# Kernel optimization log

Hardware: AMD Instinct MI355X
Metric: run time of the kernel (lower is better)

Reference implementation:

```python
import jax, jax.numpy as jnp
import numpy as np

TW = 25          # time_window
H = 128          # hidden_features
NL = 6           # hidden_layer
N = 8192         # batch*n_nodes
E = 131072       # edges (avg degree 16)
EDGE_DIM = 51    # 50 (u diff) + 1 (pos_x diff)
LEM_IN = 4       # pos_x, u_ch0, u_ch1, ts
PDE_L = 16.0
PDE_TMAX = 4.0
PDE_DT = 0.04
NEG_SLOPE = 0.2  # PyG GATConv leaky_relu slope


def swish(x):
    return x * jax.nn.sigmoid(x)


def setup_inputs() -> dict:
    key = jax.random.key(0)
    ks = jax.random.split(key, 32)
    def p(k, shape, s=0.05):
        return jax.random.normal(k, shape, jnp.float32) * s
    inp = {}
    inp['u'] = jax.random.normal(ks[0], (N, 2 * TW), jnp.float32)
    inp['pos'] = jax.random.uniform(ks[1], (N, 2), jnp.float32)
    inp['edge_index'] = jax.random.randint(ks[2], (2, E), 0, N)
    # LEM cell params (inp2hid: 4H, hid2hid: 3H, transform_z: H)
    inp['lem_inp_w'] = p(ks[3], (4 * H, LEM_IN)); inp['lem_inp_b'] = jnp.zeros(4 * H, jnp.float32)
    inp['lem_hid_w'] = p(ks[4], (3 * H, H));      inp['lem_hid_b'] = jnp.zeros(3 * H, jnp.float32)
    inp['lem_z_w'] = p(ks[5], (H, H));            inp['lem_z_b'] = jnp.zeros(H, jnp.float32)
    # lemoutput_mlp
    inp['mlp1_w'] = p(ks[6], (H, H)); inp['mlp1_b'] = jnp.zeros(H, jnp.float32)
    inp['mlp2_w'] = p(ks[7], (H, H)); inp['mlp2_b'] = jnp.zeros(H, jnp.float32)
    # main GAT layers (stacked over NL)
    inp['gnn_lin_w'] = p(ks[8], (NL, H, H)); inp['gnn_edge_w'] = p(ks[9], (NL, H, EDGE_DIM))
    inp['gnn_att_src'] = p(ks[10], (NL, H)); inp['gnn_att_dst'] = p(ks[11], (NL, H))
    inp['gnn_att_edge'] = p(ks[12], (NL, H)); inp['gnn_bias'] = jnp.zeros((NL, H), jnp.float32)
    # gate GAT layers
    inp['gate_lin_w'] = p(ks[13], (NL, H, H)); inp['gate_edge_w'] = p(ks[14], (NL, H, EDGE_DIM))
    inp['gate_att_src'] = p(ks[15], (NL, H)); inp['gate_att_dst'] = p(ks[16], (NL, H))
    inp['gate_att_edge'] = p(ks[17], (NL, H)); inp['gate_bias'] = jnp.zeros((NL, H), jnp.float32)
    # double_mlp + conv1d decoder (time_window==25 branch)
    inp['dbl_w'] = p(ks[18], (2 * H, H)); inp['dbl_b'] = jnp.zeros(2 * H, jnp.float32)
    inp['conv1_w'] = p(ks[19], (8, 2, 16)); inp['conv1_b'] = jnp.zeros(8, jnp.float32)
    inp['conv2_w'] = p(ks[20], (2, 8, 14)); inp['conv2_b'] = jnp.zeros(2, jnp.float32)
    return inp


def _gat(x, src, dst, edge_attr, lin_w, edge_w, a_src, a_dst, a_edge, bias):
    """Single-head GATConv with edge features (PyG semantics, aggregate at dst)."""
    xt = x @ lin_w.T                      # [N,H]
    et = edge_attr @ edge_w.T             # [E,H]
    logits = jax.nn.leaky_relu((xt @ a_src)[src] + (xt @ a_dst)[dst] + et @ a_edge, NEG_SLOPE)
    amax = jax.ops.segment_max(logits, dst, num_segments=N)
    amax = jnp.where(jnp.isfinite(amax), amax, 0.0)
    ex = jnp.exp(logits - amax[dst])
    denom = jax.ops.segment_sum(ex, dst, num_segments=N)
    w = ex / (denom[dst] + 1e-16)         # edge softmax over incoming edges
    out = jax.ops.segment_sum(w[:, None] * xt[src], dst, num_segments=N)
    return out + bias


def _forward(u, pos, lem_inp_w, lem_inp_b, lem_hid_w, lem_hid_b, lem_z_w, lem_z_b,
             mlp1_w, mlp1_b, mlp2_w, mlp2_b,
             gnn_lin_w, gnn_edge_w, gnn_att_src, gnn_att_dst, gnn_att_edge, gnn_bias,
             gate_lin_w, gate_edge_w, gate_att_src, gate_att_dst, gate_att_edge, gate_bias,
             dbl_w, dbl_b, conv1_w, conv1_b, conv2_w, conv2_b, edge_index):
    pos_x = pos[:, 1:2] / PDE_L    # [N,1]
    pos_t = pos[:, 0:1] / PDE_TMAX # [N,1]
    dt = jnp.cumsum(jnp.full((TW,), PDE_DT, jnp.float32))  # [TW]
    ts = pos_t + dt[None, :]       # [N,TW]
    # LEM input: [TW, N, 4] = (pos_x, u channel 0, u channel 1, ts)
    lem_x = jnp.concatenate([
        jnp.broadcast_to(pos_x[None, :, :], (TW, N, 1)),
        u[:, :TW].T[:, :, None],
        u[:, TW:].T[:, :, None],
        ts.T[:, :, None],
    ], axis=-1)

    def cell(carry, xt):
        y, z = carry
        ii = xt @ lem_inp_w.T + lem_inp_b   # [N,4H]
        hh = y @ lem_hid_w.T + lem_hid_b    # [N,3H]
        i1, i2, i3, i4 = jnp.split(ii, 4, axis=-1)
        h1, h2, h3 = jnp.split(hh, 3, axis=-1)
        ms_dt_bar = jax.nn.sigmoid(i1 + h1)
        ms_dt = jax.nn.sigmoid(i2 + h2)
        z = (1.0 - ms_dt) * z + ms_dt * jnp.tanh(i3 + h3)
        y = (1.0 - ms_dt_bar) * y + ms_dt_bar * jnp.tanh(z @ lem_z_w.T + lem_z_b + i4)
        return (y, z), None

    y0 = jnp.zeros((N, H), u.dtype)
    (y, _), _ = jax.lax.scan(cell, (y0, y0), lem_x)
    h = swish(y @ mlp1_w.T + mlp1_b)
    h = swish(h @ mlp2_w.T + mlp2_b)

    src, dst = edge_index[0], edge_index[1]
    edge_attr = jnp.concatenate([u[src] - u[dst], pos_x[src] - pos_x[dst]], axis=-1)  # [E,51]

    for i in range(NL):
        tau = jax.nn.sigmoid(_gat(h, src, dst, edge_attr, gate_lin_w[i], gate_edge_w[i],
                                  gate_att_src[i], gate_att_dst[i], gate_att_edge[i], gate_bias[i]))
        msg = swish(_gat(h, src, dst, edge_attr, gnn_lin_w[i], gnn_edge_w[i],
                         gnn_att_src[i], gnn_att_dst[i], gnn_att_edge[i], gnn_bias[i]))
        h = (1.0 - tau) * h + tau * msg

    h2 = swish(h @ dbl_w.T + dbl_b).reshape(N, 2, H)  # [N,2,128]
    dn = ('NCH', 'OIH', 'NCH')
    d = jax.lax.conv_general_dilated(h2, conv1_w, (3,), 'VALID', dimension_numbers=dn)
    d = swish(d + conv1_b[None, :, None])              # [N,8,38]
    d = jax.lax.conv_general_dilated(d, conv2_w, (1,), 'VALID', dimension_numbers=dn)
    d = d + conv2_b[None, :, None]                     # [N,2,25]
    out = u.reshape(N, 2, TW) + dt[None, None, :] * d
    return out.reshape(N, 2 * TW)


def reference(u, pos, edge_index, lem_inp_w, lem_inp_b, lem_hid_w, lem_hid_b, lem_z_w, lem_z_b,
              mlp1_w, mlp1_b, mlp2_w, mlp2_b,
              gnn_lin_w, gnn_edge_w, gnn_att_src, gnn_att_dst, gnn_att_edge, gnn_bias,
              gate_lin_w, gate_edge_w, gate_att_src, gate_att_dst, gate_att_edge, gate_bias,
              dbl_w, dbl_b, conv1_w, conv1_b, conv2_w, conv2_b):
    return _forward(u, pos, lem_inp_w, lem_inp_b, lem_hid_w, lem_hid_b, lem_z_w, lem_z_b,
                    mlp1_w, mlp1_b, mlp2_w, mlp2_b,
                    gnn_lin_w, gnn_edge_w, gnn_att_src, gnn_att_dst, gnn_att_edge, gnn_bias,
                    gate_lin_w, gate_edge_w, gate_att_src, gate_att_dst, gate_att_edge, gate_bias,
                    dbl_w, dbl_b, conv1_w, conv1_b, conv2_w, conv2_b, edge_index)
```

## Files before the change

### kernel.cpp

```cpp
#include <hip/hip_runtime.h>
#include <hip/hip_cooperative_groups.h>

#define N_NODES 8192
#define N_EDGES 131072

namespace cg = cooperative_groups;

using short8 = __attribute__((ext_vector_type(8))) short;
using f32x4  = __attribute__((ext_vector_type(4))) float;

__device__ __forceinline__ float rcpf(float x){ return __builtin_amdgcn_rcpf(x); }
__device__ __forceinline__ float sigm(float x){ return rcpf(1.0f+__expf(-x)); }
__device__ __forceinline__ float ftanh(float x){ float e=__expf(2.0f*x); return (e-1.0f)*rcpf(e+1.0f); }
__device__ __forceinline__ float swishf(float x){ return x*sigm(x); }
__device__ __forceinline__ float leaky(float x){ return x>=0.0f? x : 0.2f*x; }
__device__ __forceinline__ float dot4(float4 a, float4 b){ return a.x*b.x+a.y*b.y+a.z*b.z+a.w*b.w; }
__device__ __forceinline__ short f2bf(float x){
  unsigned u=__float_as_uint(x);
  unsigned r=(u + 0x7fffu + ((u>>16)&1u))>>16;
  return (short)r;
}
__device__ __forceinline__ int cvtpk(float a, float b){
  int r; asm("v_cvt_pk_bf16_f32 %0, %1, %2" : "=v"(r) : "v"(a), "v"(b)); return r;
}

__device__ __forceinline__ float wave_rsum(float v){
  #pragma unroll
  for(int m=32;m;m>>=1) v+=__shfl_xor(v,m);
  return v;
}

__global__ __launch_bounds__(256) void hist_kernel(const int* __restrict__ dst, int* __restrict__ cnt){
  int e=blockIdx.x*256+threadIdx.x;
  if(e<N_EDGES) atomicAdd(&cnt[dst[e]],1);
}

__global__ __launch_bounds__(1024) void scan_kernel(const int* __restrict__ cnt, int* __restrict__ rowptr, int* __restrict__ cursor){
  __shared__ int sums[1024];
  int t=threadIdx.x; int base=t*8;
  int local[8]; int s=0;
  #pragma unroll
  for(int i=0;i<8;++i){ local[i]=s; s+=cnt[base+i]; }
  sums[t]=s; __syncthreads();
  for(int off=1;off<1024;off<<=1){
    int v=(t>=off)?sums[t-off]:0;
    __syncthreads();
    sums[t]+=v;
    __syncthreads();
  }
  int offset=(t>0)?sums[t-1]:0;
  #pragma unroll
  for(int i=0;i<8;++i){ int v=offset+local[i]; rowptr[base+i]=v; cursor[base+i]=v; }
  if(t==1023) rowptr[N_NODES]=sums[1023];
}

__global__ __launch_bounds__(256) void scatter_kernel(const int* __restrict__ src, const int* __restrict__ dst,
                                                      int* __restrict__ cursor, int* __restrict__ csr_src){
  int e=blockIdx.x*256+threadIdx.x;
  if(e<N_EDGES){
    int slot=atomicAdd(&cursor[dst[e]],1);
    csr_src[slot]=src[e];
  }
}

__global__ __launch_bounds__(256) void prep_bf16_kernel(
    const float* __restrict__ lem_hid_w, const float* __restrict__ lem_z_w,
    const float* __restrict__ mlp1_w, const float* __restrict__ mlp2_w,
    const float* __restrict__ gate_lin_w, const float* __restrict__ gnn_lin_w,
    const float* __restrict__ gate_ew, const float* __restrict__ gnn_ew,
    const float* __restrict__ gate_ae, const float* __restrict__ gnn_ae,
    short* __restrict__ whb, short* __restrict__ wzb, short* __restrict__ w1b,
    short* __restrict__ w2b, short* __restrict__ wlin16, float* __restrict__ we)
{
  int i=blockIdx.x*256+threadIdx.x;
  if(i<49152){ whb[i]=f2bf(lem_hid_w[i]); return; }
  if(i<65536){ int k=i-49152; wzb[k]=f2bf(lem_z_w[k]); return; }
  if(i<81920){ int k=i-65536; w1b[k]=f2bf(mlp1_w[k]); return; }
  if(i<98304){ int k=i-81920; w2b[k]=f2bf(mlp2_w[k]); return; }
  if(i<294912){
    int k=i-98304;
    int l=k>>15, which=(k>>14)&1, r=k&16383;
    const float* s = which? gnn_lin_w + l*16384 + r : gate_lin_w + l*16384 + r;
    wlin16[k]=f2bf(*s);
    return;
  }
  int idx=i-294912;
  if(idx>=12*51) return;
  int g=idx/51, k=idx%51, l=g>>1;
  const float* ew = (g&1)? gnn_ew + l*128*51 : gate_ew + l*128*51;
  const float* ae = (g&1)? gnn_ae + l*128    : gate_ae + l*128;
  float s=0.f;
  for(int f=0;f<128;++f) s+=ew[f*51+k]*ae[f];
  we[idx]=s;
}

__global__ __launch_bounds__(128) void gsc_kernel(const float* __restrict__ u, const float* __restrict__ pos,
                                                  const float* __restrict__ we, float* __restrict__ gsc){
  int n=blockIdx.x*128+threadIdx.x;
  float uv[50];
  #pragma unroll
  for(int k=0;k<50;++k) uv[k]=u[n*50+k];
  float px=pos[n*2+1]*(1.0f/16.0f);
  for(int g=0;g<12;++g){
    const float* w=we+g*51;
    float s=w[50]*px;
    #pragma unroll
    for(int k=0;k<50;++k) s+=w[k]*uv[k];
    gsc[g*N_NODES+n]=s;
  }
}

__device__ __forceinline__ void transform_phase(
    int tid, int n0,
    const short* __restrict__ h16, short* __restrict__ xts,
    float* __restrict__ ssred, float* __restrict__ sdred,
    const short* __restrict__ wl,
    const float* __restrict__ a_sg, const float* __restrict__ a_dg,
    const float* __restrict__ a_sm, const float* __restrict__ a_dm,
    const float* __restrict__ gsc_g, const float* __restrict__ gsc_m,
    short* __restrict__ xt_out, float* __restrict__ ss_out, float* __restrict__ sd_out)
{
  const int lane=tid&63, w=tid>>6;
  const int cg_=w&1, ch=w>>1;
  const int r16=lane&15, kq=lane>>4;
  __syncthreads();
  short8 afr[4];
  #pragma unroll
  for(int kk=0;kk<4;++kk)
    afr[kk]=*(const short8*)&h16[r16*128 + ((kk*32+kq*8) ^ ((r16&7)<<3))];
  const short* wb = wl + cg_*16384;
  const float* as_ = cg_? a_sm : a_sg;
  const float* ad_ = cg_? a_dm : a_dg;
  float ssp[4]={0,0,0,0}, sdp[4]={0,0,0,0};
  #pragma unroll
  for(int ci=0;ci<2;++ci){
    int c0=(ch*2+ci)*16;
    f32x4 acc={0.f,0.f,0.f,0.f};
    #pragma unroll
    for(int kk=0;kk<4;++kk){
      short8 b=*(const short8*)(wb + (c0+r16)*128 + kk*32 + kq*8);
      acc=__builtin_amdgcn_mfma_f32_16x16x32_bf16(afr[kk],b,acc,0,0,0);
    }
    float av=as_[c0+r16], dv=ad_[c0+r16];
    #pragma unroll
    for(int r=0;r<4;++r){
      ssp[r]+=acc[r]*av; sdp[r]+=acc[r]*dv;
      xts[(kq*4+r)*256 + cg_*128 + c0 + r16]=f2bf(acc[r]);
    }
  }
  #pragma unroll
  for(int m=1;m<16;m<<=1){
    #pragma unroll
    for(int r=0;r<4;++r){ ssp[r]+=__shfl_xor(ssp[r],m); sdp[r]+=__shfl_xor(sdp[r],m); }
  }
  if(r16==0){
    #pragma unroll
    for(int r=0;r<4;++r){ ssred[w*16+kq*4+r]=ssp[r]; sdred[w*16+kq*4+r]=sdp[r]; }
  }
  __syncthreads();
  if(tid<32){
    int node=tid&15, cg2=tid>>4;
    float sv=0.f, dv=0.f;
    #pragma unroll
    for(int c2=0;c2<4;++c2){ sv+=ssred[(c2*2+cg2)*16+node]; dv+=sdred[(c2*2+cg2)*16+node]; }
    float gv=(cg2? gsc_m:gsc_g)[n0+node];
    ss_out[2*(n0+node)+cg2]=sv+gv;
    sd_out[2*(n0+node)+cg2]=dv-gv;
  }
  {
    const short8* sp=(const short8*)xts;
    short8* dp=(short8*)(xt_out + (size_t)n0*256);
    dp[tid]=sp[tid];
  }
}

__device__ __forceinline__ float4 aggregate_node(
    int n, int lane, float4* __restrict__ stgw,
    const int* __restrict__ rowptr, const int* __restrict__ csr_src,
    const short* __restrict__ xt_in, const float* __restrict__ ss_in, const float* __restrict__ sd_in,
    const float* __restrict__ bias_g, const float* __restrict__ bias_m,
    const float* __restrict__ hrow)
{
  const int s0=rowptr[n], deg=rowptr[n+1]-s0;
  const float2 sdv=*(const float2*)(sd_in+2*n);
  const float bg=sdv.x, bm=sdv.y;
  float dg=0.f,dm=0.f, acc0=0.f,acc1=0.f,acc2=0.f,acc3=0.f;
  for(int c=0;c<deg;c+=64){
    int i=c+lane, s=0; float eg=0.f, em=0.f;
    if(i<deg){
      s=csr_src[s0+i];
      float2 ssv=*(const float2*)(ss_in+2*s);
      eg=__expf(fminf(leaky(ssv.x+bg),60.f));
      em=__expf(fminf(leaky(ssv.y+bm),60.f));
      dg+=eg; dm+=em;
    }
    float4 st; st.x=__int_as_float(s); st.y=eg; st.z=em; st.w=0.f;
    stgw[lane]=st;
    __threadfence_block();
    int cnt=min(64,deg-c);
    for(int cb=0;cb<cnt;cb+=8){
      int sj[8]; float wj[8];
      #pragma unroll
      for(int j=0;j<8;++j){
        int idx=cb+j;
        float4 ev=stgw[idx<cnt? idx : cb];
        sj[j]=__float_as_int(ev.x);
        wj[j]=(idx<cnt)? (lane<32? ev.y : ev.z) : 0.f;
      }
      uint2 rows[8];
      #pragma unroll
      for(int j=0;j<8;++j)
        rows[j]=*(const uint2*)(xt_in + (size_t)sj[j]*256 + 4*lane);
      #pragma unroll
      for(int j=0;j<8;++j){
        float wv=wj[j];
        unsigned p0=rows[j].x, p1=rows[j].y;
        acc0+=wv*__uint_as_float(p0<<16);
        acc1+=wv*__uint_as_float(p0&0xffff0000u);
        acc2+=wv*__uint_as_float(p1<<16);
        acc3+=wv*__uint_as_float(p1&0xffff0000u);
      }
    }
  }
  dg=wave_rsum(dg); dm=wave_rsum(dm);
  float rr = lane<32? rcpf(dg+1e-16f) : rcpf(dm+1e-16f);
  const float* bp = lane<32? bias_g+4*lane : bias_m+4*(lane-32);
  float4 bv=*(const float4*)bp;
  float o0=acc0*rr+bv.x, o1=acc1*rr+bv.y, o2=acc2*rr+bv.z, o3=acc3*rr+bv.w;
  float s0_=sigm(o0), s1_=sigm(o1), s2_=sigm(o2), s3_=sigm(o3);
  float v0=lane<32? s0_:o0*s0_;
  float v1=lane<32? s1_:o1*s1_;
  float v2=lane<32? s2_:o2*s2_;
  float v3=lane<32? s3_:o3*s3_;
  float m0=__shfl_xor(v0,32), m1=__shfl_xor(v1,32), m2=__shfl_xor(v2,32), m3=__shfl_xor(v3,32);
  float4 r;
  if(lane<32){
    float4 hv=*(const float4*)(hrow + 4*lane);
    r.x=(1.0f-v0)*hv.x+v0*m0;
    r.y=(1.0f-v1)*hv.y+v1*m1;
    r.z=(1.0f-v2)*hv.z+v2*m2;
    r.w=(1.0f-v3)*hv.w+v3*m3;
  } else { r.x=r.y=r.z=r.w=0.f; }
  return r;
}

__global__ __launch_bounds__(512,2) void lem_t0_kernel(
    const float* __restrict__ u, const float* __restrict__ pos,
    const float* __restrict__ Wi, const float* __restrict__ bi,
    const short* __restrict__ whb, const float* __restrict__ bh,
    const short* __restrict__ wzb, const float* __restrict__ bz,
    const short* __restrict__ w1b, const float* __restrict__ b1,
    const short* __restrict__ w2b, const float* __restrict__ b2,
    float* __restrict__ hout,
    const short* __restrict__ wl,
    const float* __restrict__ a_sg, const float* __restrict__ a_dg,
    const float* __restrict__ a_sm, const float* __restrict__ a_dm,
    const float* __restrict__ gsc_g, const float* __restrict__ gsc_m,
    short* __restrict__ xt_out, float* __restrict__ ss_out, float* __restrict__ sd_out)
{
  __shared__ short y16[2][16*128];
  __shared__ short z16[2][16*128];
  __shared__ float u_s[32*50];
  __shared__ short h16[16*128];
  __shared__ short xts[16*256];
  __shared__ float ssred[128], sdred[128];

  const int tid=threadIdx.x, lane=tid&63, w=tid>>6;
  const int node=lane&15, q=lane>>4;
  const int n7=node&7;
  const int n0=blockIdx.x*32;

  for(int i=tid;i<32*50;i+=512) u_s[i]=u[n0*50+i];
  for(int i=tid;i<2*16*64;i+=512) ((int*)y16)[i]=0;

  const float px0=pos[(n0+node)*2+1]*(1.0f/16.0f),    pt0=pos[(n0+node)*2+0]*0.25f;
  const float px1=pos[(n0+16+node)*2+1]*(1.0f/16.0f), pt1=pos[(n0+16+node)*2+0]*0.25f;

  float bb[4][4], wix[4][4], wiw[4][4], wiy[4][4], wiz[4][4];
  #pragma unroll
  for(int gg=0; gg<4; ++gg){
    #pragma unroll
    for(int r=0;r<4;++r){
      int fr = w*16+q*4+r;
      int row = gg*128+fr;
      float4 wi = *(const float4*)(Wi+4*row);
      bb[gg][r] = bi[row] + ((gg<3)? bh[row] : bz[fr]);
      wix[gg][r]=wi.x; wiw[gg][r]=wi.w; wiy[gg][r]=wi.y; wiz[gg][r]=wi.z;
    }
  }

  short8 whf[3][4];
  #pragma unroll
  for(int gg=0;gg<3;++gg)
    #pragma unroll
    for(int kk=0;kk<4;++kk)
      whf[gg][kk]=*(const short8*)(whb + (gg*128 + w*16 + node)*128 + kk*32 + q*8);
  short8 wzf[4];
  #pragma unroll
  for(int kk=0;kk<4;++kk)
    wzf[kk]=*(const short8*)(wzb + (w*16 + node)*128 + kk*32 + q*8);

  float yr0[4]={0.f,0.f,0.f,0.f}, zr0[4]={0.f,0.f,0.f,0.f};
  float yr1[4]={0.f,0.f,0.f,0.f}, zr1[4]={0.f,0.f,0.f,0.f};
  float msb0[4], i4s0[4], msb1[4], i4s1[4];
  const int wrslot = (w*16+q*4) ^ (n7<<3);
  const int rdbase = n7<<3;
  __syncthreads();

  for(int t=0;t<25;++t){
    const float tf=(float)(t+1);
    {
      f32x4 h1a={0.f,0.f,0.f,0.f}, h2a=h1a, h3a=h1a;
      #pragma unroll
      for(int kk=0;kk<4;++kk){
        short8 yb=*(const short8*)&y16[0][node*128 + ((kk*32 + q*8) ^ rdbase)];
        h1a=__builtin_amdgcn_mfma_f32_16x16x32_bf16(whf[0][kk],yb,h1a,0,0,0);
        h2a=__builtin_amdgcn_mfma_f32_16x16x32_bf16(whf[1][kk],yb,h2a,0,0,0);
        h3a=__builtin_amdgcn_mfma_f32_16x16x32_bf16(whf[2][kk],yb,h3a,0,0,0);
      }
      const float u0=u_s[node*50+t], u1=u_s[node*50+25+t];
      const float ts=pt0+0.04f*tf;
      #pragma unroll
      for(int r=0;r<4;++r){
        float i1=bb[0][r]+wix[0][r]*px0+wiw[0][r]*ts+wiy[0][r]*u0+wiz[0][r]*u1;
        float i2=bb[1][r]+wix[1][r]*px0+wiw[1][r]*ts+wiy[1][r]*u0+wiz[1][r]*u1;
        float i3=bb[2][r]+wix[2][r]*px0+wiw[2][r]*ts+wiy[2][r]*u0+wiz[2][r]*u1;
        i4s0[r] =bb[3][r]+wix[3][r]*px0+wiw[3][r]*ts+wiy[3][r]*u0+wiz[3][r]*u1;
        msb0[r]=sigm(i1+h1a[r]);
        float ms=sigm(i2+h2a[r]);
        zr0[r]=(1.0f-ms)*zr0[r]+ms*ftanh(i3+h3a[r]);
      }
      int2 zz; zz.x=cvtpk(zr0[0],zr0[1]); zz.y=cvtpk(zr0[2],zr0[3]);
      *(int2*)&z16[0][node*128 + wrslot]=zz;
    }
    {
      f32x4 h1a={0.f,0.f,0.f,0.f}, h2a=h1a, h3a=h1a;
      #pragma unroll
      for(int kk=0;kk<4;++kk){
        short8 yb=*(const short8*)&y16[1][node*128 + ((kk*32 + q*8) ^ rdbase)];
        h1a=__builtin_amdgcn_mfma_f32_16x16x32_bf16(whf[0][kk],yb,h1a,0,0,0);
        h2a=__builtin_amdgcn_mfma_f32_16x16x32_bf16(whf[1][kk],yb,h2a,0,0,0);
        h3a=__builtin_amdgcn_mfma_f32_16x16x32_bf16(whf[2][kk],yb,h3a,0,0,0);
      }
      const float u0=u_s[(16+node)*50+t], u1=u_s[(16+node)*50+25+t];
      const float ts=pt1+0.04f*tf;
      #pragma unroll
      for(int r=0;r<4;++r){
        float i1=bb[0][r]+wix[0][r]*px1+wiw[0][r]*ts+wiy[0][r]*u0+wiz[0][r]*u1;
        float i2=bb[1][r]+wix[1][r]*px1+wiw[1][r]*ts+wiy[1][r]*u0+wiz[1][r]*u1;
        float i3=bb[2][r]+wix[2][r]*px1+wiw[2][r]*ts+wiy[2][r]*u0+wiz[2][r]*u1;
        i4s1[r] =bb[3][r]+wix[3][r]*px1+wiw[3][r]*ts+wiy[3][r]*u0+wiz[3][r]*u1;
        msb1[r]=sigm(i1+h1a[r]);
        float ms=sigm(i2+h2a[r]);
        zr1[r]=(1.0f-ms)*zr1[r]+ms*ftanh(i3+h3a[r]);
      }
      int2 zz; zz.x=cvtpk(zr1[0],zr1[1]); zz.y=cvtpk(zr1[2],zr1[3]);
      *(int2*)&z16[1][node*128 + wrslot]=zz;
    }
    __syncthreads();
    {
      f32x4 zw={0.f,0.f,0.f,0.f};
      #pragma unroll
      for(int kk=0;kk<4;++kk){
        short8 zb=*(const short8*)&z16[0][node*128 + ((kk*32 + q*8) ^ rdbase)];
        zw=__builtin_amdgcn_mfma_f32_16x16x32_bf16(wzf[kk],zb,zw,0,0,0);
      }
      #pragma unroll
      for(int r=0;r<4;++r)
        yr0[r]=(1.0f-msb0[r])*yr0[r]+msb0[r]*ftanh(zw[r]+i4s0[r]);
      int2 yy; yy.x=cvtpk(yr0[0],yr0[1]); yy.y=cvtpk(yr0[2],yr0[3]);
      *(int2*)&y16[0][node*128 + wrslot]=yy;
    }
    {
      f32x4 zw={0.f,0.f,0.f,0.f};
      #pragma unroll
      for(int kk=0;kk<4;++kk){
        short8 zb=*(const short8*)&z16[1][node*128 + ((kk*32 + q*8) ^ rdbase)];
        zw=__builtin_amdgcn_mfma_f32_16x16x32_bf16(wzf[kk],zb,zw,0,0,0);
      }
      #pragma unroll
      for(int r=0;r<4;++r)
        yr1[r]=(1.0f-msb1[r])*yr1[r]+msb1[r]*ftanh(zw[r]+i4s1[r]);
      int2 yy; yy.x=cvtpk(yr1[0],yr1[1]); yy.y=cvtpk(yr1[2],yr1[3]);
      *(int2*)&y16[1][node*128 + wrslot]=yy;
    }
    __syncthreads();
  }

  #pragma unroll
  for(int nt=0;nt<2;++nt){
    {
      short8 w1f[4];
      #pragma unroll
      for(int kk=0;kk<4;++kk)
        w1f[kk]=*(const short8*)(w1b + (w*16 + node)*128 + kk*32 + q*8);
      float4 b1v=*(const float4*)(b1 + w*16 + q*4);
      f32x4 a={0.f,0.f,0.f,0.f};
      #pragma unroll
      for(int kk=0;kk<4;++kk){
        short8 yb=*(const short8*)&y16[nt][node*128 + ((kk*32 + q*8) ^ rdbase)];
        a=__builtin_amdgcn_mfma_f32_16x16x32_bf16(w1f[kk],yb,a,0,0,0);
      }
      float t0=swishf(a[0]+b1v.x), t1=swishf(a[1]+b1v.y);
      float t2=swishf(a[2]+b1v.z), t3=swishf(a[3]+b1v.w);
      int2 zz; zz.x=cvtpk(t0,t1); zz.y=cvtpk(t2,t3);
      *(int2*)&z16[nt][node*128 + wrslot]=zz;
    }
    __syncthreads();
    {
      short8 w2f[4];
      #pragma unroll
      for(int kk=0;kk<4;++kk)
        w2f[kk]=*(const short8*)(w2b + (w*16 + node)*128 + kk*32 + q*8);
      float4 b2v=*(const float4*)(b2 + w*16 + q*4);
      f32x4 a={0.f,0.f,0.f,0.f};
      #pragma unroll
      for(int kk=0;kk<4;++kk){
        short8 zb=*(const short8*)&z16[nt][node*128 + ((kk*32 + q*8) ^ rdbase)];
        a=__builtin_amdgcn_mfma_f32_16x16x32_bf16(w2f[kk],zb,a,0,0,0);
      }
      float h0=swishf(a[0]+b2v.x), h1=swishf(a[1]+b2v.y);
      float h2=swishf(a[2]+b2v.z), h3=swishf(a[3]+b2v.w);
      float4 hv; hv.x=h0; hv.y=h1; hv.z=h2; hv.w=h3;
      *(float4*)(hout + (size_t)(n0+nt*16+node)*128 + w*16+q*4)=hv;
      int2 hb; hb.x=cvtpk(h0,h1); hb.y=cvtpk(h2,h3);
      *(int2*)&h16[node*128 + wrslot]=hb;
    }
    transform_phase(tid,n0+nt*16,h16,xts,ssred,sdred,wl,a_sg,a_dg,a_sm,a_dm,gsc_g,gsc_m,xt_out,ss_out,sd_out);
  }
}

__global__ __launch_bounds__(512,2) void gnn_persist_kernel(
    const int* __restrict__ rowptr, const int* __restrict__ csr_src,
    const float* __restrict__ hin,
    short* __restrict__ xtA, float* __restrict__ ssA, float* __restrict__ sdA,
    short* __restrict__ xtB, float* __restrict__ ssB, float* __restrict__ sdB,
    const short* __restrict__ wlin16,
    const float* __restrict__ gate_att_src, const float* __restrict__ gate_att_dst,
    const float* __restrict__ gnn_att_src, const float* __restrict__ gnn_att_dst,
    const float* __restrict__ gsc,
    const float* __restrict__ gate_bias, const float* __restrict__ gnn_bias,
    const float* __restrict__ u,
    const float* __restrict__ Wd, const float* __restrict__ bd,
    const float* __restrict__ w1, const float* __restrict__ b1,
    const float* __restrict__ w2, const float* __restrict__ b2,
    float* __restrict__ out)
{
  __shared__ float hfp[32*128];
  __shared__ union SM {
    struct {
      short h16[16*128];
      short xts[16*256];
      float ssred[128], sdred[128];
      float4 stg[8][64];
    } g;
    struct {
      float h2[16][2][128];
      float c1[16][8][38];
      float w1s[256], w2s[224], b1s[8], b2s[2];
    } d;
  } sm;

  cg::grid_group grid = cg::this_grid();
  const int tid=threadIdx.x, lane=tid&63, w=tid>>6;
  const int n0=blockIdx.x*32;

  for(int i=tid;i<32*128;i+=512) hfp[i]=hin[(size_t)n0*128+i];
  __syncthreads();

  for(int l=0;l<6;++l){
    const short* xt_in = (l&1)? xtB : xtA;
    const float* ss_in = (l&1)? ssB : ssA;
    const float* sd_in = (l&1)? sdB : sdA;
    const float* bias_g = gate_bias + l*128;
    const float* bias_m = gnn_bias + l*128;
    #pragma unroll
    for(int nt=0;nt<2;++nt){
      #pragma unroll
      for(int which=0;which<2;++which){
        int rl=w*2+which;
        int row=nt*16+rl;
        int n=n0+row;
        float4 hv=aggregate_node(n,lane,sm.g.stg[w],rowptr,csr_src,xt_in,ss_in,sd_in,bias_g,bias_m,&hfp[row*128]);
        if(lane<32){
          *(float4*)&hfp[row*128+4*lane]=hv;
          int2 hb; hb.x=cvtpk(hv.x,hv.y); hb.y=cvtpk(hv.z,hv.w);
          *(int2*)&sm.g.h16[rl*128 + ((4*lane) ^ ((rl&7)<<3))]=hb;
        }
      }
      if(l<5){
        int lp=l+1;
        transform_phase(tid,n0+nt*16,sm.g.h16,sm.g.xts,sm.g.ssred,sm.g.sdred,
          wlin16+(size_t)lp*32768,
          gate_att_src+lp*128, gate_att_dst+lp*128,
          gnn_att_src+lp*128, gnn_att_dst+lp*128,
          gsc+(size_t)(2*lp)*N_NODES, gsc+(size_t)(2*lp+1)*N_NODES,
          (l&1)? xtA:xtB, (l&1)? ssA:ssB, (l&1)? sdA:sdB);
      }
    }
    if(l<5){
      __threadfence();
      grid.sync();
      __threadfence();
    }
  }

  __syncthreads();
  if(tid<256) sm.d.w1s[tid]=w1[tid];
  else if(tid<480) sm.d.w2s[tid-256]=w2[tid-256];
  else if(tid<488) sm.d.b1s[tid-480]=b1[tid-480];
  else if(tid<490) sm.d.b2s[tid-488]=b2[tid-488];
  __syncthreads();
  for(int nt=0;nt<2;++nt){
    const float* hbase=&hfp[nt*16*128];
    {
      int o=tid&255, grp=tid>>8;
      const float4* wp=(const float4*)(Wd + o*128);
      float acc[8];
      #pragma unroll
      for(int n=0;n<8;++n) acc[n]=0.f;
      for(int k=0;k<32;++k){
        float4 wv=wp[k];
        #pragma unroll
        for(int n=0;n<8;++n){ float4 hval=*(const float4*)&hbase[(grp*8+n)*128+k*4]; acc[n]+=dot4(wv,hval); }
      }
      float bdv=bd[o];
      int chn=o>>7, p=o&127;
      #pragma unroll
      for(int n=0;n<8;++n) sm.d.h2[grp*8+n][chn][p]=swishf(acc[n]+bdv);
    }
    __syncthreads();
    for(int idx=tid; idx<16*8*38; idx+=512){
      int n=idx/(8*38); int r=idx%(8*38); int oc=r/38, p=r%38;
      float acc=sm.d.b1s[oc];
      const float* ww=&sm.d.w1s[oc*32];
      #pragma unroll
      for(int ic=0;ic<2;++ic)
        #pragma unroll
        for(int k=0;k<16;++k) acc+=ww[ic*16+k]*sm.d.h2[n][ic][3*p+k];
      sm.d.c1[n][oc][p]=swishf(acc);
    }
    __syncthreads();
    for(int idx=tid; idx<16*2*25; idx+=512){
      int n=idx/50; int r=idx%50; int oc=r/25, p=r%25;
      float acc=sm.d.b2s[oc];
      const float* ww=&sm.d.w2s[oc*112];
      #pragma unroll
      for(int ic=0;ic<8;++ic)
        #pragma unroll
        for(int k=0;k<14;++k) acc+=ww[ic*14+k]*sm.d.c1[n][ic][p+k];
      int col=oc*25+p;
      int gn=n0+nt*16+n;
      out[gn*50+col]=u[gn*50+col]+0.04f*(float)(p+1)*acc;
    }
    __syncthreads();
  }
}

__global__ __launch_bounds__(512,2) void gat_fused_kernel(
    const int* __restrict__ rowptr, const int* __restrict__ csr_src,
    const short* __restrict__ xt_in, const float* __restrict__ ss_in, const float* __restrict__ sd_in,
    const float* __restrict__ bias_g, const float* __restrict__ bias_m,
    float* __restrict__ h,
    const short* __restrict__ wl,
    const float* __restrict__ a_sg, const float* __restrict__ a_dg,
    const float* __restrict__ a_sm, const float* __restrict__ a_dm,
    const float* __restrict__ gsc_g, const float* __restrict__ gsc_m,
    short* __restrict__ xt_out, float* __restrict__ ss_out, float* __restrict__ sd_out)
{
  __shared__ short h16[16*128];
  __shared__ short xts[16*256];
  __shared__ float ssred[128], sdred[128];
  __shared__ float4 stg[8][64];
  const int tid=threadIdx.x, lane=tid&63, w=tid>>6;
  const int n0=blockIdx.x*16;
  #pragma unroll
  for(int which=0;which<2;++which){
    int row=w*2+which, n=n0+row;
    float4 hv=aggregate_node(n,lane,stg[w],rowptr,csr_src,xt_in,ss_in,sd_in,bias_g,bias_m,h+(size_t)n*128);
    if(lane<32){
      *(float4*)(h+(size_t)n*128+4*lane)=hv;
      int2 hb; hb.x=cvtpk(hv.x,hv.y); hb.y=cvtpk(hv.z,hv.w);
      *(int2*)&h16[row*128 + ((4*lane) ^ ((row&7)<<3))]=hb;
    }
  }
  transform_phase(tid,n0,h16,xts,ssred,sdred,wl,a_sg,a_dg,a_sm,a_dm,gsc_g,gsc_m,xt_out,ss_out,sd_out);
}

__global__ __launch_bounds__(512,2) void gat_last_decoder_kernel(
    const int* __restrict__ rowptr, const int* __restrict__ csr_src,
    const short* __restrict__ xt_in, const float* __restrict__ ss_in, const float* __restrict__ sd_in,
    const float* __restrict__ bias_g, const float* __restrict__ bias_m,
    const float* __restrict__ h, const float* __restrict__ u,
    const float* __restrict__ Wd, const float* __restrict__ bd,
    const float* __restrict__ w1, const float* __restrict__ b1,
    const float* __restrict__ w2, const float* __restrict__ b2,
    float* __restrict__ out)
{
  __shared__ float hdec[16*128];
  __shared__ float h2[16][2][128];
  __shared__ float c1[16][8][38];
  __shared__ float w1s[256], w2s[224], b1s[8], b2s[2];
  __shared__ float4 stg[8][64];
  const int tid=threadIdx.x, lane=tid&63, w=tid>>6;
  const int n0=blockIdx.x*16;
  if(tid<256) w1s[tid]=w1[tid];
  else if(tid<480) w2s[tid-256]=w2[tid-256];
  else if(tid<488) b1s[tid-480]=b1[tid-480];
  else if(tid<490) b2s[tid-488]=b2[tid-488];
  #pragma unroll
  for(int which=0;which<2;++which){
    int row=w*2+which, n=n0+row;
    float4 hv=aggregate_node(n,lane,stg[w],rowptr,csr_src,xt_in,ss_in,sd_in,bias_g,bias_m,h+(size_t)n*128);
    if(lane<32) *(float4*)&hdec[row*128+4*lane]=hv;
  }
  __syncthreads();
  {
    int o=tid&255, grp=tid>>8;
    const float4* wp=(const float4*)(Wd + o*128);
    float acc[8];
    #pragma unroll
    for(int n=0;n<8;++n) acc[n]=0.f;
    for(int k=0;k<32;++k){
      float4 wv=wp[k];
      #pragma unroll
      for(int n=0;n<8;++n){ float4 hval=*(const float4*)&hdec[(grp*8+n)*128+k*4]; acc[n]+=dot4(wv,hval); }
    }
    float bdv=bd[o];
    int chn=o>>7, p=o&127;
    #pragma unroll
    for(int n=0;n<8;++n) h2[grp*8+n][chn][p]=swishf(acc[n]+bdv);
  }
  __syncthreads();
  for(int idx=tid; idx<16*8*38; idx+=512){
    int n=idx/(8*38); int r=idx%(8*38); int oc=r/38, p=r%38;
    float acc=b1s[oc];
    const float* ww=&w1s[oc*32];
    #pragma unroll
    for(int ic=0;ic<2;++ic)
      #pragma unroll
      for(int k=0;k<16;++k) acc+=ww[ic*16+k]*h2[n][ic][3*p+k];
    c1[n][oc][p]=swishf(acc);
  }
  __syncthreads();
  for(int idx=tid; idx<16*2*25; idx+=512){
    int n=idx/50; int r=idx%50; int oc=r/25, p=r%25;
    float acc=b2s[oc];
    const float* ww=&w2s[oc*112];
    #pragma unroll
    for(int ic=0;ic<8;++ic)
      #pragma unroll
      for(int k=0;k<14;++k) acc+=ww[ic*14+k]*c1[n][ic][p+k];
    int col=oc*25+p;
    out[(n0+n)*50+col]=u[(n0+n)*50+col]+0.04f*(float)(p+1)*acc;
  }
}

extern "C" void kernel_launch(void* const* d_in, const int* in_sizes, int n_in,
                              void* d_out, int out_size, void* d_ws, size_t ws_size,
                              hipStream_t stream)
{
  const float* u          =(const float*)d_in[0];
  const float* pos        =(const float*)d_in[1];
  const int*   ei         =(const int*)d_in[2];
  const float* lem_inp_w  =(const float*)d_in[3];
  const float* lem_inp_b  =(const float*)d_in[4];
  const float* lem_hid_w  =(const float*)d_in[5];
  const float* lem_hid_b  =(const float*)d_in[6];
  const float* lem_z_w    =(const float*)d_in[7];
  const float* lem_z_b    =(const float*)d_in[8];
  const float* mlp1_w     =(const float*)d_in[9];
  const float* mlp1_b     =(const float*)d_in[10];
  const float* mlp2_w     =(const float*)d_in[11];
  const float* mlp2_b     =(const float*)d_in[12];
  const float* gnn_lin_w  =(const float*)d_in[13];
  const float* gnn_edge_w =(const float*)d_in[14];
  const float* gnn_att_src=(const float*)d_in[15];
  const float* gnn_att_dst=(const float*)d_in[16];
  const float* gnn_att_edge=(const float*)d_in[17];
  const float* gnn_bias   =(const float*)d_in[18];
  const float* gate_lin_w =(const float*)d_in[19];
  const float* gate_edge_w=(const float*)d_in[20];
  const float* gate_att_src=(const float*)d_in[21];
  const float* gate_att_dst=(const float*)d_in[22];
  const float* gate_att_edge=(const float*)d_in[23];
  const float* gate_bias  =(const float*)d_in[24];
  const float* dbl_w      =(const float*)d_in[25];
  const float* dbl_b      =(const float*)d_in[26];
  const float* conv1_w    =(const float*)d_in[27];
  const float* conv1_b    =(const float*)d_in[28];
  const float* conv2_w    =(const float*)d_in[29];
  const float* conv2_b    =(const float*)d_in[30];
  float* out=(float*)d_out;

  char* ws=(char*)d_ws;
  size_t off=0;
  auto alloc=[&](size_t bytes)->char*{ char* p=ws+off; off+=(bytes+255)&~(size_t)255; return p; };
  float* h    =(float*)alloc((size_t)N_NODES*128*4);
  short* xtA  =(short*)alloc((size_t)N_NODES*256*2);
  short* xtB  =(short*)alloc((size_t)N_NODES*256*2);
  float* ssA  =(float*)alloc((size_t)N_NODES*2*4);
  float* ssB  =(float*)alloc((size_t)N_NODES*2*4);
  float* sdA  =(float*)alloc((size_t)N_NODES*2*4);
  float* sdB  =(float*)alloc((size_t)N_NODES*2*4);
  float* gsc  =(float*)alloc((size_t)12*N_NODES*4);
  float* wearr=(float*)alloc(12*51*4);
  int* cnt    =(int*)alloc(N_NODES*4);
  int* rowptr =(int*)alloc((N_NODES+8)*4);
  int* cursor =(int*)alloc(N_NODES*4);
  int* csrsrc =(int*)alloc((size_t)N_EDGES*4);
  short* whb  =(short*)alloc(384*128*2);
  short* wzb  =(short*)alloc(128*128*2);
  short* w1b  =(short*)alloc(128*128*2);
  short* w2b  =(short*)alloc(128*128*2);
  short* wlin16=(short*)alloc((size_t)6*2*128*128*2);

  const int* src=ei;
  const int* dst=ei+N_EDGES;

  hipMemsetAsync(cnt,0,N_NODES*4,stream);
  hist_kernel<<<N_EDGES/256,256,0,stream>>>(dst,cnt);
  scan_kernel<<<1,1024,0,stream>>>(cnt,rowptr,cursor);
  scatter_kernel<<<N_EDGES/256,256,0,stream>>>(src,dst,cursor,csrsrc);
  prep_bf16_kernel<<<(294912+612+255)/256,256,0,stream>>>(lem_hid_w,lem_z_w,mlp1_w,mlp2_w,
                                                      gate_lin_w,gnn_lin_w,
                                                      gate_edge_w,gnn_edge_w,gate_att_edge,gnn_att_edge,
                                                      whb,wzb,w1b,w2b,wlin16,wearr);
  gsc_kernel<<<N_NODES/128,128,0,stream>>>(u,pos,wearr,gsc);

  lem_t0_kernel<<<N_NODES/32,512,0,stream>>>(u,pos,lem_inp_w,lem_inp_b,whb,lem_hid_b,
      wzb,lem_z_b,w1b,mlp1_b,w2b,mlp2_b,h,
      wlin16,
      gate_att_src, gate_att_dst, gnn_att_src, gnn_att_dst,
      gsc, gsc+(size_t)N_NODES,
      xtA, ssA, sdA);

  int occ=0;
  hipError_t qerr=hipOccupancyMaxActiveBlocksPerMultiprocessor(&occ,
      reinterpret_cast<const void*>(gnn_persist_kernel), 512, 0);
  bool coop = (qerr==hipSuccess) && (occ>=1);

  if(coop){
    void* kargs[]={
      (void*)&rowptr,(void*)&csrsrc,(void*)&h,
      (void*)&xtA,(void*)&ssA,(void*)&sdA,
      (void*)&xtB,(void*)&ssB,(void*)&sdB,
      (void*)&wlin16,
      (void*)&gate_att_src,(void*)&gate_att_dst,(void*)&gnn_att_src,(void*)&gnn_att_dst,
      (void*)&gsc,
      (void*)&gate_bias,(void*)&gnn_bias,
      (void*)&u,(void*)&dbl_w,(void*)&dbl_b,
      (void*)&conv1_w,(void*)&conv1_b,(void*)&conv2_w,(void*)&conv2_b,
      (void*)&out
    };
    hipError_t lerr=hipLaunchCooperativeKernel((void*)gnn_persist_kernel,
        dim3(N_NODES/32), dim3(512), kargs, 0, stream);
    if(lerr==hipSuccess) return;
  }

  for(int l=0;l<5;++l){
    short* xin = (l&1)? xtB:xtA;  float* sin_=(l&1)? ssA:ssA;
    (void)xin; (void)sin_;
  }
  {
    short* xtbuf[2]={xtA,xtB};
    float* ssbuf[2]={ssA,ssB};
    float* sdbuf[2]={sdA,sdB};
    for(int l=0;l<5;++l){
      int in=l&1, o2=(l+1)&1;
      gat_fused_kernel<<<N_NODES/16,512,0,stream>>>(rowptr,csrsrc,
        xtbuf[in],ssbuf[in],sdbuf[in],
        gate_bias+l*128, gnn_bias+l*128, h,
        wlin16+(size_t)(l+1)*2*16384,
        gate_att_src+(l+1)*128, gate_att_dst+(l+1)*128,
        gnn_att_src+(l+1)*128, gnn_att_dst+(l+1)*128,
        gsc+(size_t)(2*(l+1))*N_NODES, gsc+(size_t)(2*(l+1)+1)*N_NODES,
        xtbuf[o2], ssbuf[o2], sdbuf[o2]);
    }
    gat_last_decoder_kernel<<<N_NODES/16,512,0,stream>>>(rowptr,csrsrc,
        xtbuf[1],ssbuf[1],sdbuf[1],
        gate_bias+5*128, gnn_bias+5*128, h, u,
        dbl_w, dbl_b, conv1_w, conv1_b, conv2_w, conv2_b, out);
  }
}
```

Measured before the change: 356.8 us.

## Halve nodes per persistent block, raise occupancy, and reorder gather before weight computation

The cooperative persistent GNN kernel now gives each block 16 nodes instead of 32, doubles the grid to 512 blocks, and sets launch bounds to 4 blocks per SM, which requires occupancy of at least 2 for the cooperative path. The aggregation loop stages source indices first and issues 16 row gathers per batch before computing the attention exponentials. This lets the exp/score latency overlap the outstanding gathers. It also splits the LDS staging into separate index and weight arrays. The tighter launch bounds may cause register spills, and if occupancy drops below 2 the code falls back to the multi-kernel path.

```diff
diff --git a/kernel.cpp b/kernel.cpp
--- a/kernel.cpp
+++ b/kernel.cpp
@@ -175,7 +175,7 @@
 }
 
 __device__ __forceinline__ float4 aggregate_node(
-    int n, int lane, float4* __restrict__ stgw,
+    int n, int lane, int* __restrict__ sidx, float2* __restrict__ wstg,
     const int* __restrict__ rowptr, const int* __restrict__ csr_src,
     const short* __restrict__ xt_in, const float* __restrict__ ss_in, const float* __restrict__ sd_in,
     const float* __restrict__ bias_g, const float* __restrict__ bias_m,
@@ -186,34 +186,36 @@
   const float bg=sdv.x, bm=sdv.y;
   float dg=0.f,dm=0.f, acc0=0.f,acc1=0.f,acc2=0.f,acc3=0.f;
   for(int c=0;c<deg;c+=64){
-    int i=c+lane, s=0; float eg=0.f, em=0.f;
-    if(i<deg){
-      s=csr_src[s0+i];
-      float2 ssv=*(const float2*)(ss_in+2*s);
-      eg=__expf(fminf(leaky(ssv.x+bg),60.f));
-      em=__expf(fminf(leaky(ssv.y+bm),60.f));
-      dg+=eg; dm+=em;
-    }
-    float4 st; st.x=__int_as_float(s); st.y=eg; st.z=em; st.w=0.f;
-    stgw[lane]=st;
+    int i=c+lane, s=0;
+    bool act=(i<deg);
+    if(act) s=csr_src[s0+i];
+    sidx[lane]= act? s : 0;
     __threadfence_block();
     int cnt=min(64,deg-c);
-    for(int cb=0;cb<cnt;cb+=8){
-      int sj[8]; float wj[8];
-      #pragma unroll
-      for(int j=0;j<8;++j){
+    for(int cb=0;cb<cnt;cb+=16){
+      uint2 rows[16];
+      #pragma unroll
+      for(int j=0;j<16;++j){
         int idx=cb+j;
-        float4 ev=stgw[idx<cnt? idx : cb];
-        sj[j]=__float_as_int(ev.x);
-        wj[j]=(idx<cnt)? (lane<32? ev.y : ev.z) : 0.f;
-      }
-      uint2 rows[8];
-      #pragma unroll
-      for(int j=0;j<8;++j)
-        rows[j]=*(const uint2*)(xt_in + (size_t)sj[j]*256 + 4*lane);
-      #pragma unroll
-      for(int j=0;j<8;++j){
-        float wv=wj[j];
+        int sj=sidx[idx<cnt? idx : cb];
+        rows[j]=*(const uint2*)(xt_in + (size_t)sj*256 + 4*lane);
+      }
+      if(cb==0){
+        float eg=0.f, em=0.f;
+        if(act){
+          float2 ssv=*(const float2*)(ss_in+2*s);
+          eg=__expf(fminf(leaky(ssv.x+bg),60.f));
+          em=__expf(fminf(leaky(ssv.y+bm),60.f));
+          dg+=eg; dm+=em;
+        }
+        wstg[lane]=make_float2(eg,em);
+        __threadfence_block();
+      }
+      #pragma unroll
+      for(int j=0;j<16;++j){
+        int idx=cb+j;
+        float2 wv2=wstg[idx<cnt? idx : cb];
+        float wv=(idx<cnt)? (lane<32? wv2.x : wv2.y) : 0.f;
         unsigned p0=rows[j].x, p1=rows[j].y;
         acc0+=wv*__uint_as_float(p0<<16);
         acc1+=wv*__uint_as_float(p0&0xffff0000u);
@@ -430,7 +432,7 @@
   }
 }
 
-__global__ __launch_bounds__(512,2) void gnn_persist_kernel(
+__global__ __launch_bounds__(512,4) void gnn_persist_kernel(
     const int* __restrict__ rowptr, const int* __restrict__ csr_src,
     const float* __restrict__ hin,
     short* __restrict__ xtA, float* __restrict__ ssA, float* __restrict__ sdA,
@@ -446,13 +448,14 @@
     const float* __restrict__ w2, const float* __restrict__ b2,
     float* __restrict__ out)
 {
-  __shared__ float hfp[32*128];
+  __shared__ float hfp[16*128];
   __shared__ union SM {
     struct {
       short h16[16*128];
       short xts[16*256];
       float ssred[128], sdred[128];
-      float4 stg[8][64];
+      int sidx[8][64];
+      float2 wstg[8][64];
     } g;
     struct {
       float h2[16][2][128];
@@ -463,9 +466,9 @@
 
   cg::grid_group grid = cg::this_grid();
   const int tid=threadIdx.x, lane=tid&63, w=tid>>6;
-  const int n0=blockIdx.x*32;
-
-  for(int i=tid;i<32*128;i+=512) hfp[i]=hin[(size_t)n0*128+i];
+  const int n0=blockIdx.x*16;
+
+  for(int i=tid;i<16*128;i+=512) hfp[i]=hin[(size_t)n0*128+i];
   __syncthreads();
 
   for(int l=0;l<6;++l){
@@ -475,30 +478,24 @@
     const float* bias_g = gate_bias + l*128;
     const float* bias_m = gnn_bias + l*128;
     #pragma unroll
-    for(int nt=0;nt<2;++nt){
-      #pragma unroll
-      for(int which=0;which<2;++which){
-        int rl=w*2+which;
-        int row=nt*16+rl;
-        int n=n0+row;
-        float4 hv=aggregate_node(n,lane,sm.g.stg[w],rowptr,csr_src,xt_in,ss_in,sd_in,bias_g,bias_m,&hfp[row*128]);
-        if(lane<32){
-          *(float4*)&hfp[row*128+4*lane]=hv;
-          int2 hb; hb.x=cvtpk(hv.x,hv.y); hb.y=cvtpk(hv.z,hv.w);
-          *(int2*)&sm.g.h16[rl*128 + ((4*lane) ^ ((rl&7)<<3))]=hb;
-        }
-      }
-      if(l<5){
-        int lp=l+1;
-        transform_phase(tid,n0+nt*16,sm.g.h16,sm.g.xts,sm.g.ssred,sm.g.sdred,
-          wlin16+(size_t)lp*32768,
-          gate_att_src+lp*128, gate_att_dst+lp*128,
-          gnn_att_src+lp*128, gnn_att_dst+lp*128,
-          gsc+(size_t)(2*lp)*N_NODES, gsc+(size_t)(2*lp+1)*N_NODES,
-          (l&1)? xtA:xtB, (l&1)? ssA:ssB, (l&1)? sdA:sdB);
+    for(int which=0;which<2;++which){
+      int row=w*2+which, n=n0+row;
+      float4 hv=aggregate_node(n,lane,sm.g.sidx[w],sm.g.wstg[w],
+                               rowptr,csr_src,xt_in,ss_in,sd_in,bias_g,bias_m,&hfp[row*128]);
+      if(lane<32){
+        *(float4*)&hfp[row*128+4*lane]=hv;
+        int2 hb; hb.x=cvtpk(hv.x,hv.y); hb.y=cvtpk(hv.z,hv.w);
+        *(int2*)&sm.g.h16[row*128 + ((4*lane) ^ ((row&7)<<3))]=hb;
       }
     }
     if(l<5){
+      int lp=l+1;
+      transform_phase(tid,n0,sm.g.h16,sm.g.xts,sm.g.ssred,sm.g.sdred,
+        wlin16+(size_t)lp*32768,
+        gate_att_src+lp*128, gate_att_dst+lp*128,
+        gnn_att_src+lp*128, gnn_att_dst+lp*128,
+        gsc+(size_t)(2*lp)*N_NODES, gsc+(size_t)(2*lp+1)*N_NODES,
+        (l&1)? xtA:xtB, (l&1)? ssA:ssB, (l&1)? sdA:sdB);
       __threadfence();
       grid.sync();
       __threadfence();
@@ -511,49 +508,45 @@
   else if(tid<488) sm.d.b1s[tid-480]=b1[tid-480];
   else if(tid<490) sm.d.b2s[tid-488]=b2[tid-488];
   __syncthreads();
-  for(int nt=0;nt<2;++nt){
-    const float* hbase=&hfp[nt*16*128];
-    {
-      int o=tid&255, grp=tid>>8;
-      const float4* wp=(const float4*)(Wd + o*128);
-      float acc[8];
-      #pragma unroll
-      for(int n=0;n<8;++n) acc[n]=0.f;
-      for(int k=0;k<32;++k){
-        float4 wv=wp[k];
-        #pragma unroll
-        for(int n=0;n<8;++n){ float4 hval=*(const float4*)&hbase[(grp*8+n)*128+k*4]; acc[n]+=dot4(wv,hval); }
-      }
-      float bdv=bd[o];
-      int chn=o>>7, p=o&127;
-      #pragma unroll
-      for(int n=0;n<8;++n) sm.d.h2[grp*8+n][chn][p]=swishf(acc[n]+bdv);
-    }
-    __syncthreads();
-    for(int idx=tid; idx<16*8*38; idx+=512){
-      int n=idx/(8*38); int r=idx%(8*38); int oc=r/38, p=r%38;
-      float acc=sm.d.b1s[oc];
-      const float* ww=&sm.d.w1s[oc*32];
-      #pragma unroll
-      for(int ic=0;ic<2;++ic)
-        #pragma unroll
-        for(int k=0;k<16;++k) acc+=ww[ic*16+k]*sm.d.h2[n][ic][3*p+k];
-      sm.d.c1[n][oc][p]=swishf(acc);
-    }
-    __syncthreads();
-    for(int idx=tid; idx<16*2*25; idx+=512){
-      int n=idx/50; int r=idx%50; int oc=r/25, p=r%25;
-      float acc=sm.d.b2s[oc];
-      const float* ww=&sm.d.w2s[oc*112];
-      #pragma unroll
-      for(int ic=0;ic<8;++ic)
-        #pragma unroll
-        for(int k=0;k<14;++k) acc+=ww[ic*14+k]*sm.d.c1[n][ic][p+k];
-      int col=oc*25+p;
-      int gn=n0+nt*16+n;
-      out[gn*50+col]=u[gn*50+col]+0.04f*(float)(p+1)*acc;
-    }
-    __syncthreads();
+  {
+    int o=tid&255, grp=tid>>8;
+    const float4* wp=(const float4*)(Wd + o*128);
+    float acc[8];
+    #pragma unroll
+    for(int n=0;n<8;++n) acc[n]=0.f;
+    for(int k=0;k<32;++k){
+      float4 wv=wp[k];
+      #pragma unroll
+      for(int n=0;n<8;++n){ float4 hval=*(const float4*)&hfp[(grp*8+n)*128+k*4]; acc[n]+=dot4(wv,hval); }
+    }
+    float bdv=bd[o];
+    int chn=o>>7, p=o&127;
+    #pragma unroll
+    for(int n=0;n<8;++n) sm.d.h2[grp*8+n][chn][p]=swishf(acc[n]+bdv);
+  }
+  __syncthreads();
+  for(int idx=tid; idx<16*8*38; idx+=512){
+    int n=idx/(8*38); int r=idx%(8*38); int oc=r/38, p=r%38;
+    float acc=sm.d.b1s[oc];
+    const float* ww=&sm.d.w1s[oc*32];
+    #pragma unroll
+    for(int ic=0;ic<2;++ic)
+      #pragma unroll
+      for(int k=0;k<16;++k) acc+=ww[ic*16+k]*sm.d.h2[n][ic][3*p+k];
+    sm.d.c1[n][oc][p]=swishf(acc);
+  }
+  __syncthreads();
+  for(int idx=tid; idx<16*2*25; idx+=512){
+    int n=idx/50; int r=idx%50; int oc=r/25, p=r%25;
+    float acc=sm.d.b2s[oc];
+    const float* ww=&sm.d.w2s[oc*112];
+    #pragma unroll
+    for(int ic=0;ic<8;++ic)
+      #pragma unroll
+      for(int k=0;k<14;++k) acc+=ww[ic*14+k]*sm.d.c1[n][ic][p+k];
+    int col=oc*25+p;
+    int gn=n0+n;
+    out[gn*50+col]=u[gn*50+col]+0.04f*(float)(p+1)*acc;
   }
 }
 
@@ -571,13 +564,14 @@
   __shared__ short h16[16*128];
   __shared__ short xts[16*256];
   __shared__ float ssred[128], sdred[128];
-  __shared__ float4 stg[8][64];
+  __shared__ int sidx[8][64];
+  __shared__ float2 wstg[8][64];
   const int tid=threadIdx.x, lane=tid&63, w=tid>>6;
   const int n0=blockIdx.x*16;
   #pragma unroll
   for(int which=0;which<2;++which){
     int row=w*2+which, n=n0+row;
-    float4 hv=aggregate_node(n,lane,stg[w],rowptr,csr_src,xt_in,ss_in,sd_in,bias_g,bias_m,h+(size_t)n*128);
+    float4 hv=aggregate_node(n,lane,sidx[w],wstg[w],rowptr,csr_src,xt_in,ss_in,sd_in,bias_g,bias_m,h+(size_t)n*128);
     if(lane<32){
       *(float4*)(h+(size_t)n*128+4*lane)=hv;
       int2 hb; hb.x=cvtpk(hv.x,hv.y); hb.y=cvtpk(hv.z,hv.w);
@@ -601,7 +595,8 @@
   __shared__ float h2[16][2][128];
   __shared__ float c1[16][8][38];
   __shared__ float w1s[256], w2s[224], b1s[8], b2s[2];
-  __shared__ float4 stg[8][64];
+  __shared__ int sidx[8][64];
+  __shared__ float2 wstg[8][64];
   const int tid=threadIdx.x, lane=tid&63, w=tid>>6;
   const int n0=blockIdx.x*16;
   if(tid<256) w1s[tid]=w1[tid];
@@ -611,7 +606,7 @@
   #pragma unroll
   for(int which=0;which<2;++which){
     int row=w*2+which, n=n0+row;
-    float4 hv=aggregate_node(n,lane,stg[w],rowptr,csr_src,xt_in,ss_in,sd_in,bias_g,bias_m,h+(size_t)n*128);
+    float4 hv=aggregate_node(n,lane,sidx[w],wstg[w],rowptr,csr_src,xt_in,ss_in,sd_in,bias_g,bias_m,h+(size_t)n*128);
     if(lane<32) *(float4*)&hdec[row*128+4*lane]=hv;
   }
   __syncthreads();
@@ -738,7 +733,7 @@
   int occ=0;
   hipError_t qerr=hipOccupancyMaxActiveBlocksPerMultiprocessor(&occ,
       reinterpret_cast<const void*>(gnn_persist_kernel), 512, 0);
-  bool coop = (qerr==hipSuccess) && (occ>=1);
+  bool coop = (qerr==hipSuccess) && (occ>=2);
 
   if(coop){
     void* kargs[]={
@@ -754,14 +749,10 @@
       (void*)&out
     };
     hipError_t lerr=hipLaunchCooperativeKernel((void*)gnn_persist_kernel,
-        dim3(N_NODES/32), dim3(512), kargs, 0, stream);
+        dim3(N_NODES/16), dim3(512), kargs, 0, stream);
     if(lerr==hipSuccess) return;
   }
 
-  for(int l=0;l<5;++l){
-    short* xin = (l&1)? xtB:xtA;  float* sin_=(l&1)? ssA:ssA;
-    (void)xin; (void)sin_;
-  }
   {
     short* xtbuf[2]={xtA,xtB};
     float* ssbuf[2]={ssA,ssB};
```

New measurement: 368.0 us. 1.03x slower.
